# Optimization experiments

Hardware: AMD Instinct MI355X
Metric: run time of the kernel (lower is better)

## Reference

```python
import jax, jax.numpy as jnp
import numpy as np

B, LAT, CIN, W, K, F = 16, 512, 512, 4096, 3, 512

def setup_inputs() -> dict:
    key = jax.random.key(0)
    k1, k2, k3, k4 = jax.random.split(key, 4)
    latent = jax.random.normal(k1, (B, LAT), jnp.float32)
    content = jax.random.normal(k2, (B, CIN, W), jnp.float32)
    # glorot_uniform for affine weight
    lim = np.sqrt(6.0 / (LAT + CIN))
    affine_w = jax.random.uniform(k3, (LAT, CIN), jnp.float32, -lim, lim)
    affine_b = jnp.zeros((1, CIN), jnp.float32)
    # he_normal for conv kernel (fan_in = K*CIN)
    kernel_w = jax.random.normal(k4, (K, CIN, F), jnp.float32) * np.sqrt(2.0 / (K * CIN))
    kernel_b = jnp.zeros((1, F, 1), jnp.float32)
    return {"latent": latent, "content": content, "affine_w": affine_w,
            "affine_b": affine_b, "kernel_w": kernel_w, "kernel_b": kernel_b}

def reference(latent, content, affine_w, affine_b, kernel_w, kernel_b):
    # style affine: [B, CIN]
    affine = latent @ affine_w + affine_b
    # demod scale per (b, f): 1/sqrt(sum_{k,c} (kernel[k,c,f]*affine[b,c])^2 + 1e-8)
    demod = jax.lax.rsqrt(jnp.einsum('kcf,bc->bf', kernel_w * kernel_w,
                                     affine * affine) + 1e-8)
    # modulate input instead of per-sample weights (mathematically identical,
    # avoids batch-as-groups grouped conv): x[b,c,w] = content * affine[b,c]
    x = content * affine[:, :, None]
    # shared-kernel conv1d, NCW / SAME; filter layout [K, CIN, F] == HIO
    y = jax.lax.conv_general_dilated(
        x, kernel_w, window_strides=(1,), padding='SAME',
        dimension_numbers=('NCH', 'HIO', 'NCH'))
    y = y * demod[:, :, None] + kernel_b  # [B, F, W]
    return jnp.where(y >= 0, y, 0.2 * y)  # leaky_relu(0.2)
```

## Files before the change

### kernel.cpp

```cpp
#include <hip/hip_runtime.h>
#include <hip/hip_bf16.h>

#define Bn   16
#define LATn 512
#define Cn   512
#define Wn   4096
#define Fn   512

using bf16x8 = __attribute__((ext_vector_type(8))) short;
using f32x4  = __attribute__((ext_vector_type(4))) float;

__device__ __forceinline__ unsigned short f2bf(float x) {
    union { float f; unsigned int u; } v; v.f = x;
    unsigned int r = v.u + 0x7fffu + ((v.u >> 16) & 1u);
    return (unsigned short)(r >> 16);
}

__device__ __forceinline__ void gload_lds16(const void* g, void* l) {
    __builtin_amdgcn_global_load_lds(
        (const __attribute__((address_space(1))) unsigned int*)g,
        (__attribute__((address_space(3))) unsigned int*)l, 16, 0, 0);
}

__global__ void k_affine(const float* __restrict__ latent,
                         const float* __restrict__ aw,
                         const float* __restrict__ ab,
                         float* __restrict__ affine,
                         float* __restrict__ zbuf) {
    if (blockIdx.x == 0 && blockIdx.y == 0 && threadIdx.x < 16)
        zbuf[threadIdx.x] = 0.f;
    __shared__ float red[4][64];
    const int t  = threadIdx.x;
    const int cl = t & 63, lq = t >> 6;
    const int c  = blockIdx.x * 64 + cl;
    const int b  = blockIdx.y;
    float s = 0.f;
    #pragma unroll 4
    for (int l = lq * 128; l < lq * 128 + 128; ++l)
        s = fmaf(latent[b * LATn + l], aw[(size_t)l * Cn + c], s);
    red[lq][cl] = s;
    __syncthreads();
    if (t < 64)
        affine[b * Cn + blockIdx.x * 64 + t] =
            red[0][t] + red[1][t] + red[2][t] + red[3][t] + ab[blockIdx.x * 64 + t];
}

__global__ __launch_bounds__(256)
void k_mid(const float* __restrict__ kw,
           const float* __restrict__ affine,
           const float* __restrict__ content,
           float* __restrict__ demod,
           unsigned short* __restrict__ kt,
           unsigned short* __restrict__ xt) {
    __shared__ __align__(16) char shraw[9216];
    const int t   = threadIdx.x;
    const int bid = blockIdx.x;

    if (bid < 128) {
        float (*red)[64] = (float(*)[64])shraw;
        const int fl = t & 63, cq = t >> 6;
        const int f  = (bid & 7) * 64 + fl;
        const int b  = bid >> 3;
        float s = 0.f;
        for (int c = cq * 128; c < cq * 128 + 128; ++c) {
            const float a  = affine[b * Cn + c];
            const float k0 = kw[((size_t)(0 * Cn + c)) * Fn + f];
            const float k1 = kw[((size_t)(1 * Cn + c)) * Fn + f];
            const float k2 = kw[((size_t)(2 * Cn + c)) * Fn + f];
            s = fmaf(k0 * k0 + k1 * k1 + k2 * k2, a * a, s);
        }
        red[cq][fl] = s;
        __syncthreads();
        if (t < 64)
            demod[b * Fn + (bid & 7) * 64 + t] =
                rsqrtf(red[0][t] + red[1][t] + red[2][t] + red[3][t] + 1e-8f);
    } else if (bid < 512) {
        float (*lds)[65] = (float(*)[65])shraw;
        const int e  = bid - 128;
        const int k  = e / 128;
        const int e2 = e % 128;
        const int c0 = (e2 & 15) * 32;
        const int f0 = (e2 >> 4) * 64;
        #pragma unroll
        for (int i = 0; i < 8; ++i) {
            int q = t + 256 * i; int c = q >> 6; int f = q & 63;
            lds[c][f] = kw[((size_t)(k * Cn + c0 + c)) * Fn + f0 + f];
        }
        __syncthreads();
        #pragma unroll
        for (int i = 0; i < 8; ++i) {
            int q = t + 256 * i; int f = q >> 5; int c = q & 31;
            kt[((size_t)(k * Fn + f0 + f)) * Cn + c0 + c] = f2bf(lds[c][f]);
        }
    } else {
        unsigned short (*lds)[72] = (unsigned short(*)[72])shraw;
        const int e  = bid - 512;
        const int w0 = (e & 63) * 64;
        const int c0 = ((e >> 6) & 7) * 64;
        const int b  = e >> 9;
        #pragma unroll
        for (int i = 0; i < 4; ++i) {
            int q = t + 256 * i;
            int c = q >> 4;
            int w4 = (q & 15) * 4;
            float4 v = *(const float4*)&content[((size_t)(b * Cn + c0 + c)) * Wn + w0 + w4];
            float a = affine[b * Cn + c0 + c];
            int wx = w4 ^ ((c >> 3) << 3);
            unsigned short p[4] = {f2bf(v.x * a), f2bf(v.y * a), f2bf(v.z * a), f2bf(v.w * a)};
            *(uint2*)&lds[c][wx] = *(const uint2*)p;
        }
        __syncthreads();
        #pragma unroll
        for (int i = 0; i < 2; ++i) {
            int q  = t + 256 * i;
            int w  = q >> 3;
            int qq = q & 7;
            int c8 = qq * 8;
            int wx = w ^ (qq << 3);
            unsigned short tmp[8];
            #pragma unroll
            for (int j = 0; j < 8; ++j) tmp[j] = lds[c8 + j][wx];
            *(uint4*)&xt[((size_t)b * Wn + w0 + w) * Cn + c0 + c8] = *(uint4*)tmp;
        }
    }
}

#define BM 256
#define BN 256
#define BK 32
#define KBYTES (3 * BM * BK * 2)
#define BUFB   (KBYTES + BN * BK * 2)
#define SMEMB  (2 * BUFB + 2 * Cn * 2)

extern __shared__ __align__(16) char smem[];

#define ISSUE_XT(dst, c0s) { \
    _Pragma("unroll") for (int i_ = 0; i_ < 2; ++i_) { \
        const int Q_ = i_ * 512 + t; \
        const int r_ = Q_ >> 2; \
        const int j_ = (Q_ & 3) ^ ((r_ >> 1) & 3); \
        gload_lds16(&xt[((size_t)b * Wn + w0 + r_) * Cn + (c0s) + j_ * 8], \
                    (dst) + KBYTES + (size_t)Q_ * 16); } }

#define ISSUE_PLANE(dst, c0s, P) { \
    _Pragma("unroll") for (int i_ = 0; i_ < 2; ++i_) { \
        const int Q_ = i_ * 512 + t; \
        const int r_ = (Q_ >> 2) & 255; \
        const int j_ = (Q_ & 3) ^ ((r_ >> 1) & 3); \
        gload_lds16(&kt[((size_t)((P) * Fn + f0 + r_)) * Cn + (c0s) + j_ * 8], \
                    (dst) + (size_t)((P) * 1024 + Q_) * 16); } }

#define PHASE(K, VM, ...) { \
    asm volatile("s_waitcnt vmcnt(" #VM ")" ::: "memory"); \
    asm volatile("s_barrier" ::: "memory"); \
    bf16x8 af[8]; bf16x8 bv[4]; \
    _Pragma("unroll") for (int m_ = 0; m_ < 8; ++m_) { \
        const int r_ = wm * 128 + m_ * 16 + l15; \
        af[m_] = *(const bf16x8*)(ka + ((K) * 256 + r_) * 32 + (lhi ^ ((r_ >> 1) & 3)) * 8); } \
    _Pragma("unroll") for (int n_ = 0; n_ < 4; ++n_) { \
        const int rl_ = wn * 64 + n_ * 16 + l15 + (K) - 1; \
        const unsigned short* bp_ = xa + rl_ * 32 + (lhi ^ ((rl_ >> 1) & 3)) * 8; \
        if ((K) == 0 && n_ == 0 && rl_ < 0)   bp_ = halo + c0 + lhi * 8; \
        if ((K) == 2 && n_ == 3 && rl_ > 255) bp_ = halo + 512 + c0 + lhi * 8; \
        bv[n_] = *(const bf16x8*)bp_; } \
    __VA_ARGS__; \
    asm volatile("s_waitcnt lgkmcnt(0)" ::: "memory"); \
    __builtin_amdgcn_sched_barrier(0); \
    __builtin_amdgcn_s_setprio(1); \
    _Pragma("unroll") for (int n_ = 0; n_ < 4; ++n_) \
        _Pragma("unroll") for (int m_ = 0; m_ < 8; ++m_) \
            acc[m_][n_] = __builtin_amdgcn_mfma_f32_16x16x32_bf16(af[m_], bv[n_], acc[m_][n_], 0, 0, 0); \
    __builtin_amdgcn_s_setprio(0); }

__global__ __launch_bounds__(512, 1)
void k_conv(const unsigned short* __restrict__ kt,
            const unsigned short* __restrict__ xt,
            const float* __restrict__ demod,
            const float* __restrict__ kb,
            const float* __restrict__ zbuf,
            float* __restrict__ y) {
    const int t  = threadIdx.x;
    const int w0 = blockIdx.x * BN;
    const int f0 = blockIdx.y * BM;
    const int b  = blockIdx.z;

    const int wave = t >> 6;
    const int lane = t & 63;
    const int wm   = wave >> 2;
    const int wn   = wave & 3;
    const int l15  = lane & 15;
    const int lhi  = lane >> 4;

    unsigned short* halo = (unsigned short*)(smem + 2 * BUFB);

    f32x4 acc[8][4];
    #pragma unroll
    for (int m = 0; m < 8; ++m)
        #pragma unroll
        for (int n = 0; n < 4; ++n)
            #pragma unroll
            for (int r = 0; r < 4; ++r)
                acc[m][n][r] = 0.f;

    if (t < 128) {
        const int h  = t >> 6;
        const int wg = h ? (w0 + BN) : (w0 - 1);
        const unsigned short* src = ((unsigned)wg < (unsigned)Wn)
            ? &xt[((size_t)b * Wn + wg) * Cn + (t & 63) * 8]
            : (const unsigned short*)zbuf;
        gload_lds16(src, halo + (size_t)t * 8);
    }
    ISSUE_XT(smem, 0);
    ISSUE_PLANE(smem, 0, 0);
    ISSUE_PLANE(smem, 0, 1);
    ISSUE_PLANE(smem, 0, 2);

    int cur = 0;
    for (int cc = 0; cc < Cn / BK - 1; ++cc) {
        const unsigned short* ka = (const unsigned short*)(smem + cur * BUFB);
        const unsigned short* xa = ka + 3 * BM * BK;
        char* nbuf = smem + (cur ^ 1) * BUFB;
        const int c0 = cc * BK;
        const int c1 = c0 + BK;
        PHASE(0, 4, ISSUE_XT(nbuf, c1); ISSUE_PLANE(nbuf, c1, 0);)
        PHASE(1, 6, ISSUE_PLANE(nbuf, c1, 1);)
        PHASE(2, 6, ISSUE_PLANE(nbuf, c1, 2);)
        cur ^= 1;
    }
    {
        const unsigned short* ka = (const unsigned short*)(smem + cur * BUFB);
        const unsigned short* xa = ka + 3 * BM * BK;
        const int c0 = Cn - BK;
        PHASE(0, 4, )
        PHASE(1, 2, )
        PHASE(2, 0, )
    }

    #pragma unroll
    for (int m = 0; m < 8; ++m) {
        const int fb = f0 + wm * 128 + m * 16 + lhi * 4;
        const float4 dmv = *(const float4*)&demod[b * Fn + fb];
        const float4 kbv = *(const float4*)&kb[fb];
        const float dmf[4] = {dmv.x, dmv.y, dmv.z, dmv.w};
        const float kbf[4] = {kbv.x, kbv.y, kbv.z, kbv.w};
        #pragma unroll
        for (int n = 0; n < 4; ++n) {
            const int w = w0 + wn * 64 + n * 16 + l15;
            #pragma unroll
            for (int r = 0; r < 4; ++r) {
                float v = fmaf(acc[m][n][r], dmf[r], kbf[r]);
                v = (v >= 0.f) ? v : 0.2f * v;
                y[((size_t)(b * Fn + fb + r)) * Wn + w] = v;
            }
        }
    }
}

extern "C" void kernel_launch(void* const* d_in, const int* in_sizes, int n_in,
                              void* d_out, int out_size, void* d_ws, size_t ws_size,
                              hipStream_t stream) {
    const float* latent  = (const float*)d_in[0];
    const float* content = (const float*)d_in[1];
    const float* aw      = (const float*)d_in[2];
    const float* ab      = (const float*)d_in[3];
    const float* kw      = (const float*)d_in[4];
    const float* kb      = (const float*)d_in[5];
    float* y = (float*)d_out;

    char* ws = (char*)d_ws;
    float*          affine = (float*)(ws);
    float*          demod  = (float*)(ws + 32768);
    float*          zbuf   = (float*)(ws + 65536);
    unsigned short* kt     = (unsigned short*)(ws + 131072);
    unsigned short* xt     = (unsigned short*)(ws + 2u * 1024u * 1024u);
    if (ws_size < 2u * 1024u * 1024u + (size_t)Bn * Wn * Cn * 2u) return;

    hipFuncSetAttribute((const void*)k_conv,
                        hipFuncAttributeMaxDynamicSharedMemorySize, SMEMB);

    k_affine<<<dim3(Cn / 64, Bn),                        256, 0, stream>>>(latent, aw, ab, affine, zbuf);
    k_mid   <<<dim3(128 + 384 + Wn / 64 * Cn / 64 * Bn), 256, 0, stream>>>(kw, affine, content, demod, kt, xt);
    k_conv  <<<dim3(Wn / BN, Fn / BM, Bn),               512, SMEMB, stream>>>(kt, xt, demod, kb, zbuf, y);
}
```

Measured before the change: 154.4 us.

## Restructure conv main loop to one barrier per chunk with tap-level prefetch

Replaces the three-phase per-chunk schedule, which had a vmcnt wait and barrier before each kernel tap, with a single wait and barrier per channel chunk. The whole next chunk (activations plus all three weight planes) is issued at once. LDS fragments for the next tap are read while the MFMAs of the previous tap run, and the peeled last iteration is folded into the loop. It also raises launch bounds to two blocks per CU. The aim is to cut barrier stalls and hide LDS latency. The cost is more live fragment registers under a tighter register cap, which risks spills, and a coarser overlap of global loads with compute.

```diff
diff --git a/kernel.cpp b/kernel.cpp
--- a/kernel.cpp
+++ b/kernel.cpp
@@ -150,29 +150,33 @@
         gload_lds16(&kt[((size_t)((P) * Fn + f0 + r_)) * Cn + (c0s) + j_ * 8], \
                     (dst) + (size_t)((P) * 1024 + Q_) * 16); } }
 
-#define PHASE(K, VM, ...) { \
-    asm volatile("s_waitcnt vmcnt(" #VM ")" ::: "memory"); \
-    asm volatile("s_barrier" ::: "memory"); \
-    bf16x8 af[8]; bf16x8 bv[4]; \
+#define ISSUE_ALL(dst, c0s) { \
+    ISSUE_XT(dst, c0s); \
+    ISSUE_PLANE(dst, c0s, 0); \
+    ISSUE_PLANE(dst, c0s, 1); \
+    ISSUE_PLANE(dst, c0s, 2); }
+
+#define READ_AF(K, AF) { \
     _Pragma("unroll") for (int m_ = 0; m_ < 8; ++m_) { \
         const int r_ = wm * 128 + m_ * 16 + l15; \
-        af[m_] = *(const bf16x8*)(ka + ((K) * 256 + r_) * 32 + (lhi ^ ((r_ >> 1) & 3)) * 8); } \
+        AF[m_] = *(const bf16x8*)(ka + ((K) * 256 + r_) * 32 + (lhi ^ ((r_ >> 1) & 3)) * 8); } }
+
+#define READ_BV(K, BV) { \
     _Pragma("unroll") for (int n_ = 0; n_ < 4; ++n_) { \
         const int rl_ = wn * 64 + n_ * 16 + l15 + (K) - 1; \
         const unsigned short* bp_ = xa + rl_ * 32 + (lhi ^ ((rl_ >> 1) & 3)) * 8; \
         if ((K) == 0 && n_ == 0 && rl_ < 0)   bp_ = halo + c0 + lhi * 8; \
         if ((K) == 2 && n_ == 3 && rl_ > 255) bp_ = halo + 512 + c0 + lhi * 8; \
-        bv[n_] = *(const bf16x8*)bp_; } \
-    __VA_ARGS__; \
-    asm volatile("s_waitcnt lgkmcnt(0)" ::: "memory"); \
-    __builtin_amdgcn_sched_barrier(0); \
+        BV[n_] = *(const bf16x8*)bp_; } }
+
+#define MFMA_TAP(AF, BV) { \
     __builtin_amdgcn_s_setprio(1); \
     _Pragma("unroll") for (int n_ = 0; n_ < 4; ++n_) \
         _Pragma("unroll") for (int m_ = 0; m_ < 8; ++m_) \
-            acc[m_][n_] = __builtin_amdgcn_mfma_f32_16x16x32_bf16(af[m_], bv[n_], acc[m_][n_], 0, 0, 0); \
+            acc[m_][n_] = __builtin_amdgcn_mfma_f32_16x16x32_bf16(AF[m_], BV[n_], acc[m_][n_], 0, 0, 0); \
     __builtin_amdgcn_s_setprio(0); }
 
-__global__ __launch_bounds__(512, 1)
+__global__ __launch_bounds__(512, 2)
 void k_conv(const unsigned short* __restrict__ kt,
             const unsigned short* __restrict__ xt,
             const float* __restrict__ demod,
@@ -210,30 +214,26 @@
             : (const unsigned short*)zbuf;
         gload_lds16(src, halo + (size_t)t * 8);
     }
-    ISSUE_XT(smem, 0);
-    ISSUE_PLANE(smem, 0, 0);
-    ISSUE_PLANE(smem, 0, 1);
-    ISSUE_PLANE(smem, 0, 2);
+    ISSUE_ALL(smem, 0);
 
     int cur = 0;
-    for (int cc = 0; cc < Cn / BK - 1; ++cc) {
+    for (int cc = 0; cc < Cn / BK; ++cc) {
         const unsigned short* ka = (const unsigned short*)(smem + cur * BUFB);
         const unsigned short* xa = ka + 3 * BM * BK;
         char* nbuf = smem + (cur ^ 1) * BUFB;
         const int c0 = cc * BK;
-        const int c1 = c0 + BK;
-        PHASE(0, 4, ISSUE_XT(nbuf, c1); ISSUE_PLANE(nbuf, c1, 0);)
-        PHASE(1, 6, ISSUE_PLANE(nbuf, c1, 1);)
-        PHASE(2, 6, ISSUE_PLANE(nbuf, c1, 2);)
+        asm volatile("s_waitcnt vmcnt(0)" ::: "memory");
+        asm volatile("s_barrier" ::: "memory");
+        if (cc < Cn / BK - 1) ISSUE_ALL(nbuf, c0 + BK);
+
+        bf16x8 af0[8], af1[8], af2[8], bv0[4], bv1[4], bv2[4];
+        READ_AF(0, af0); READ_BV(0, bv0);
+        READ_AF(1, af1); READ_BV(1, bv1);
+        MFMA_TAP(af0, bv0);
+        READ_AF(2, af2); READ_BV(2, bv2);
+        MFMA_TAP(af1, bv1);
+        MFMA_TAP(af2, bv2);
         cur ^= 1;
-    }
-    {
-        const unsigned short* ka = (const unsigned short*)(smem + cur * BUFB);
-        const unsigned short* xa = ka + 3 * BM * BK;
-        const int c0 = Cn - BK;
-        PHASE(0, 4, )
-        PHASE(1, 2, )
-        PHASE(2, 0, )
     }
 
     #pragma unroll
```

Result: slower. 162.5 us (+5.2%).

## Fuse content modulation and bf16 transpose into conv kernel, drop xt intermediate

Applied to the files above, without the earlier changes.

The conv kernel now reads fp32 content directly, scales it by affine from LDS, converts to bf16 and writes the transposed tile into LDS itself. This removes the separate pass that wrote and re-read a full [B,W,C] bf16 copy of the modulated input. Only the halo columns are still precomputed in k_mid. In exchange the conv main loop takes on register-staged global loads, conversion ALU work and LDS stores, and the waitcnt schedule is rearranged. The content reads are strided across channels, and each content element is read twice because there are two F-blocks.

```diff
diff --git a/kernel.cpp b/kernel.cpp
--- a/kernel.cpp
+++ b/kernel.cpp
@@ -25,10 +25,7 @@
 __global__ void k_affine(const float* __restrict__ latent,
                          const float* __restrict__ aw,
                          const float* __restrict__ ab,
-                         float* __restrict__ affine,
-                         float* __restrict__ zbuf) {
-    if (blockIdx.x == 0 && blockIdx.y == 0 && threadIdx.x < 16)
-        zbuf[threadIdx.x] = 0.f;
+                         float* __restrict__ affine) {
     __shared__ float red[4][64];
     const int t  = threadIdx.x;
     const int cl = t & 63, lq = t >> 6;
@@ -51,7 +48,7 @@
            const float* __restrict__ content,
            float* __restrict__ demod,
            unsigned short* __restrict__ kt,
-           unsigned short* __restrict__ xt) {
+           unsigned short* __restrict__ xh) {
     __shared__ __align__(16) char shraw[9216];
     const int t   = threadIdx.x;
     const int bid = blockIdx.x;
@@ -93,34 +90,19 @@
             kt[((size_t)(k * Fn + f0 + f)) * Cn + c0 + c] = f2bf(lds[c][f]);
         }
     } else {
-        unsigned short (*lds)[72] = (unsigned short(*)[72])shraw;
         const int e  = bid - 512;
-        const int w0 = (e & 63) * 64;
-        const int c0 = ((e >> 6) & 7) * 64;
-        const int b  = e >> 9;
+        const int b  = e >> 4;
+        const int wb = e & 15;
         #pragma unroll
         for (int i = 0; i < 4; ++i) {
-            int q = t + 256 * i;
-            int c = q >> 4;
-            int w4 = (q & 15) * 4;
-            float4 v = *(const float4*)&content[((size_t)(b * Cn + c0 + c)) * Wn + w0 + w4];
-            float a = affine[b * Cn + c0 + c];
-            int wx = w4 ^ ((c >> 3) << 3);
-            unsigned short p[4] = {f2bf(v.x * a), f2bf(v.y * a), f2bf(v.z * a), f2bf(v.w * a)};
-            *(uint2*)&lds[c][wx] = *(const uint2*)p;
-        }
-        __syncthreads();
-        #pragma unroll
-        for (int i = 0; i < 2; ++i) {
-            int q  = t + 256 * i;
-            int w  = q >> 3;
-            int qq = q & 7;
-            int c8 = qq * 8;
-            int wx = w ^ (qq << 3);
-            unsigned short tmp[8];
-            #pragma unroll
-            for (int j = 0; j < 8; ++j) tmp[j] = lds[c8 + j][wx];
-            *(uint4*)&xt[((size_t)b * Wn + w0 + w) * Cn + c0 + c8] = *(uint4*)tmp;
+            const int idx = t + 256 * i;
+            const int h   = idx >> 9;
+            const int c   = idx & 511;
+            const int wg  = wb * 256 + (h ? 256 : -1);
+            float v = 0.f;
+            if ((unsigned)wg < (unsigned)Wn)
+                v = content[((size_t)(b * Cn + c)) * Wn + wg] * affine[b * Cn + c];
+            xh[(((size_t)(b * 16 + wb)) * 2 + h) * 512 + c] = f2bf(v);
         }
     }
 }
@@ -128,19 +110,27 @@
 #define BM 256
 #define BN 256
 #define BK 32
-#define KBYTES (3 * BM * BK * 2)
-#define BUFB   (KBYTES + BN * BK * 2)
-#define SMEMB  (2 * BUFB + 2 * Cn * 2)
+#define KBYTES   (3 * BM * BK * 2)
+#define BUFB     (KBYTES + BN * BK * 2)
+#define HALO_OFF (2 * BUFB)
+#define ALDS_OFF (HALO_OFF + 2048)
+#define SMEMB    (ALDS_OFF + 2048)
 
 extern __shared__ __align__(16) char smem[];
 
-#define ISSUE_XT(dst, c0s) { \
+#define LOAD_C(c0s) { \
+    _Pragma("unroll") for (int j_ = 0; j_ < 16; ++j_) \
+        cbuf[j_] = content[((size_t)(b * Cn + (c0s) + cg * 16 + j_)) * Wn + w0 + wq]; }
+
+#define WRITE_X(dst, c0s) { \
+    const float* al_ = (const float*)(smem + ALDS_OFF) + (c0s) + cg * 16; \
+    unsigned short h_[16]; \
+    _Pragma("unroll") for (int j_ = 0; j_ < 16; ++j_) \
+        h_[j_] = f2bf(cbuf[j_] * al_[j_]); \
     _Pragma("unroll") for (int i_ = 0; i_ < 2; ++i_) { \
-        const int Q_ = i_ * 512 + t; \
-        const int r_ = Q_ >> 2; \
-        const int j_ = (Q_ & 3) ^ ((r_ >> 1) & 3); \
-        gload_lds16(&xt[((size_t)b * Wn + w0 + r_) * Cn + (c0s) + j_ * 8], \
-                    (dst) + KBYTES + (size_t)Q_ * 16); } }
+        const int jj_ = cg * 2 + i_; \
+        *(uint4*)((dst) + KBYTES + (size_t)wq * 64 + ((jj_ ^ ((wq >> 1) & 3)) * 16)) \
+            = *(const uint4*)(h_ + i_ * 8); } }
 
 #define ISSUE_PLANE(dst, c0s, P) { \
     _Pragma("unroll") for (int i_ = 0; i_ < 2; ++i_) { \
@@ -174,10 +164,11 @@
 
 __global__ __launch_bounds__(512, 1)
 void k_conv(const unsigned short* __restrict__ kt,
-            const unsigned short* __restrict__ xt,
+            const float* __restrict__ content,
+            const float* __restrict__ affine,
+            const unsigned short* __restrict__ xh,
             const float* __restrict__ demod,
             const float* __restrict__ kb,
-            const float* __restrict__ zbuf,
             float* __restrict__ y) {
     const int t  = threadIdx.x;
     const int w0 = blockIdx.x * BN;
@@ -190,8 +181,10 @@
     const int wn   = wave & 3;
     const int l15  = lane & 15;
     const int lhi  = lane >> 4;
-
-    unsigned short* halo = (unsigned short*)(smem + 2 * BUFB);
+    const int cg   = t >> 8;
+    const int wq   = t & 255;
+
+    unsigned short* halo = (unsigned short*)(smem + HALO_OFF);
 
     f32x4 acc[8][4];
     #pragma unroll
@@ -202,18 +195,26 @@
             for (int r = 0; r < 4; ++r)
                 acc[m][n][r] = 0.f;
 
+    float cbuf[16];
+
+    {
+        float av = affine[b * Cn + t];
+        ((float*)(smem + ALDS_OFF))[t] = av;
+    }
+    asm volatile("s_waitcnt lgkmcnt(0)" ::: "memory");
+    asm volatile("s_barrier" ::: "memory");
     if (t < 128) {
-        const int h  = t >> 6;
-        const int wg = h ? (w0 + BN) : (w0 - 1);
-        const unsigned short* src = ((unsigned)wg < (unsigned)Wn)
-            ? &xt[((size_t)b * Wn + wg) * Cn + (t & 63) * 8]
-            : (const unsigned short*)zbuf;
-        gload_lds16(src, halo + (size_t)t * 8);
-    }
-    ISSUE_XT(smem, 0);
+        const int h = t >> 6, c8 = (t & 63) * 8;
+        gload_lds16(&xh[(((size_t)(b * 16 + blockIdx.x)) * 2 + h) * 512 + c8],
+                    halo + (size_t)h * 512 + c8);
+    }
+    LOAD_C(0);
     ISSUE_PLANE(smem, 0, 0);
     ISSUE_PLANE(smem, 0, 1);
     ISSUE_PLANE(smem, 0, 2);
+    asm volatile("s_waitcnt vmcnt(6)" ::: "memory");
+    WRITE_X(smem, 0);
+    asm volatile("s_waitcnt lgkmcnt(0)" ::: "memory");
 
     int cur = 0;
     for (int cc = 0; cc < Cn / BK - 1; ++cc) {
@@ -222,9 +223,9 @@
         char* nbuf = smem + (cur ^ 1) * BUFB;
         const int c0 = cc * BK;
         const int c1 = c0 + BK;
-        PHASE(0, 4, ISSUE_XT(nbuf, c1); ISSUE_PLANE(nbuf, c1, 0);)
-        PHASE(1, 6, ISSUE_PLANE(nbuf, c1, 1);)
-        PHASE(2, 6, ISSUE_PLANE(nbuf, c1, 2);)
+        PHASE(0, 4,  LOAD_C(c1);)
+        PHASE(1, 18, ISSUE_PLANE(nbuf, c1, 0); ISSUE_PLANE(nbuf, c1, 1);)
+        PHASE(2, 4,  ISSUE_PLANE(nbuf, c1, 2); WRITE_X(nbuf, c1);)
         cur ^= 1;
     }
     {
@@ -270,15 +271,14 @@
     char* ws = (char*)d_ws;
     float*          affine = (float*)(ws);
     float*          demod  = (float*)(ws + 32768);
-    float*          zbuf   = (float*)(ws + 65536);
     unsigned short* kt     = (unsigned short*)(ws + 131072);
-    unsigned short* xt     = (unsigned short*)(ws + 2u * 1024u * 1024u);
-    if (ws_size < 2u * 1024u * 1024u + (size_t)Bn * Wn * Cn * 2u) return;
+    unsigned short* xh     = (unsigned short*)(ws + 2u * 1024u * 1024u);
+    if (ws_size < 3u * 1024u * 1024u) return;
 
     hipFuncSetAttribute((const void*)k_conv,
                         hipFuncAttributeMaxDynamicSharedMemorySize, SMEMB);
 
-    k_affine<<<dim3(Cn / 64, Bn),                        256, 0, stream>>>(latent, aw, ab, affine, zbuf);
-    k_mid   <<<dim3(128 + 384 + Wn / 64 * Cn / 64 * Bn), 256, 0, stream>>>(kw, affine, content, demod, kt, xt);
-    k_conv  <<<dim3(Wn / BN, Fn / BM, Bn),               512, SMEMB, stream>>>(kt, xt, demod, kb, zbuf, y);
-}
+    k_affine<<<dim3(Cn / 64, Bn),          256, 0, stream>>>(latent, aw, ab, affine);
+    k_mid   <<<dim3(128 + 384 + 256),      256, 0, stream>>>(kw, affine, content, demod, kt, xh);
+    k_conv  <<<dim3(Wn / BN, Fn / BM, Bn), 512, SMEMB, stream>>>(kt, content, affine, xh, demod, kb, y);
+}
```

New measurement: 146.0 us. -5.4%, faster.
